# Optimization experiments

Hardware: AMD Instinct MI355X
Metric: run time of the kernel (lower is better)

The kernel has to match this reference:

```python
import jax, jax.numpy as jnp
from jax import lax
import numpy as np

# model dims
N, CIN, T = 4, 1, 8000
C = 256      # encoder/bottleneck channels
D = 512      # dconv_size
K = 3        # residual kernel size
FK, FS = 20, 10  # front kernel / stride
REPEATS, BLOCKS = 4, 8
NB = REPEATS * BLOCKS
EPS = 1e-5
DN = ('NCH', 'OIH', 'NCH')


def setup_inputs() -> dict:
    key = jax.random.key(0)
    ks = jax.random.split(key, 20)
    rn = lambda k, s, sc=0.05: (jax.random.normal(k, s, dtype=jnp.float32) * sc)
    inp = {
        'x': jax.random.normal(ks[0], (N, CIN, T), dtype=jnp.float32),
        'w_enc': rn(ks[1], (C, CIN, FK), 0.2),
        'w1': rn(ks[2], (NB, D, C, 1)),
        'wd': rn(ks[3], (NB, D, 1, K), 0.2),
        'w2': rn(ks[4], (NB, C, D, 1)),
        'w_dec': rn(ks[5], (C, CIN, FK), 0.2),
    }
    # BatchNorm params (inference-style): bn1 over C, bn2/bn3 over D
    for name, ch, base in (('bn1', C, 6), ('bn2', D, 10), ('bn3', D, 14)):
        inp[name + '_g'] = 1.0 + rn(ks[base + 0], (NB, ch), 0.1)
        inp[name + '_b'] = rn(ks[base + 1], (NB, ch), 0.1)
        inp[name + '_m'] = rn(ks[base + 2], (NB, ch), 0.1)
        inp[name + '_v'] = 0.5 + jax.random.uniform(ks[base + 3], (NB, ch), dtype=jnp.float32)
    return inp


def _bn(x, g, b, m, v):
    # x: [N, C, L]; per-channel affine normalization (eval-mode BatchNorm1d)
    scale = g / jnp.sqrt(v + EPS)
    return x * scale[:, None] + (b - m * scale)[:, None]


def _conv1x1(x, w):
    # x: [N, Ci, L], w: [Co, Ci, 1]
    return jnp.einsum('ncl,oc->nol', x, w[:, :, 0])


def reference(x, w_enc, w1, wd, w2, w_dec,
              bn1_g, bn1_b, bn1_m, bn1_v,
              bn2_g, bn2_b, bn2_m, bn2_v,
              bn3_g, bn3_b, bn3_m, bn3_v):
    time = x.shape[2]
    # encoder: Conv1d(CIN->C, k=FK, stride=FS, padding=FK)
    xe = lax.conv_general_dilated(x, w_enc, (FS,), [(FK, FK)], dimension_numbers=DN)
    h = xe
    for i in range(NB):
        dil = 2 ** (i % BLOCKS)
        pad = dil * (K - 1) // 2
        r = _bn(h, bn1_g[i], bn1_b[i], bn1_m[i], bn1_v[i])
        r = _conv1x1(r, w1[i])                      # [N, D, L]
        r = _bn(r, bn2_g[i], bn2_b[i], bn2_m[i], bn2_v[i])
        r = lax.conv_general_dilated(r, wd[i], (1,), [(pad, pad)],
                                     rhs_dilation=(dil,), dimension_numbers=DN,
                                     feature_group_count=D)
        r = _bn(r, bn3_g[i], bn3_b[i], bn3_m[i], bn3_v[i])
        r = _conv1x1(r, w2[i])                      # [N, C, L]
        h = h + r
    mask = jax.nn.sigmoid(h)
    y = xe * mask
    # ConvTranspose1d(C->CIN, k=FK, stride=FS, padding=0)
    wk = jnp.flip(jnp.swapaxes(w_dec, 0, 1), -1)     # [CIN, C, FK]
    out = lax.conv_general_dilated(y, wk, (1,), [(FK - 1, FK - 1)],
                                   lhs_dilation=(FS,), dimension_numbers=DN)
    return out[:, :, FK:time + FK]
```

## Files before the change

kernel.cpp:

```cpp
#include <hip/hip_runtime.h>
#include <cstddef>
#include <cstring>

#define T_     8000
#define L_     803
#define C_     256
#define D_     512
#define NB_    32
#define FK_    20
#define NBATCH 4
#define EPS_   1e-5f

#define NVALID 208
#define NGRID  224
#define NTHR   512
#define SG     1040

typedef __attribute__((ext_vector_type(8))) short bf16x8;
typedef __attribute__((ext_vector_type(4))) short shortx4;
typedef __attribute__((ext_vector_type(4))) float f32x4;
typedef unsigned long long u64;

__device__ __forceinline__ short f2bf(float x) {
  unsigned u = __float_as_uint(x);
  u += 0x7FFF + ((u >> 16) & 1);
  return (short)(u >> 16);
}
__device__ __forceinline__ float bf2f(short u) {
  return __uint_as_float(((unsigned)(unsigned short)u) << 16);
}

__device__ __forceinline__ void astore8(void* p, u64 v) {
  __hip_atomic_store((u64*)p, v, __ATOMIC_RELAXED, __HIP_MEMORY_SCOPE_AGENT);
}

struct __align__(64) Bar { unsigned cnt; unsigned phase; unsigned pad[14]; };

__device__ __forceinline__ void bar_heavy(Bar* b, unsigned nblk, int tid) {
  __syncthreads();
  if (tid == 0) {
    __threadfence();
    unsigned ph = __hip_atomic_load(&b->phase, __ATOMIC_RELAXED, __HIP_MEMORY_SCOPE_AGENT);
    unsigned prev = __hip_atomic_fetch_add(&b->cnt, 1u, __ATOMIC_RELAXED, __HIP_MEMORY_SCOPE_AGENT);
    if (prev == nblk - 1) {
      __hip_atomic_store(&b->cnt, 0u, __ATOMIC_RELAXED, __HIP_MEMORY_SCOPE_AGENT);
      __hip_atomic_store(&b->phase, ph + 1u, __ATOMIC_RELEASE, __HIP_MEMORY_SCOPE_AGENT);
    } else {
      while (__hip_atomic_load(&b->phase, __ATOMIC_RELAXED, __HIP_MEMORY_SCOPE_AGENT) == ph)
        __builtin_amdgcn_s_sleep(2);
    }
    __threadfence();
  }
  __syncthreads();
}

struct KParams {
  const float *x, *w_enc, *w1, *wd, *w2, *w_dec;
  const float *g1, *bb1, *m1, *v1;
  const float *g2, *bb2, *m2, *v2;
  const float *g3, *bb3, *m3, *v3;
  float *out;
  float *s1, *o1, *s2, *o2, *s3, *o3;
  float *yb;
  short *w1b, *w2b;
  unsigned short *zg;
  unsigned short *b1b;
  unsigned *ct;
  Bar *gbar;
};

__global__ __launch_bounds__(256) void prep_kernel(KParams p) {
  const int gtid = blockIdx.x * 256 + threadIdx.x;
  const int stride = gridDim.x * 256;
  for (int i = gtid; i < NB_ * C_; i += stride) {
    float s = p.g1[i] * rsqrtf(p.v1[i] + EPS_);
    p.s1[i] = s; p.o1[i] = p.bb1[i] - p.m1[i] * s;
  }
  for (int i = gtid; i < NB_ * D_; i += stride) {
    float s2 = p.g2[i] * rsqrtf(p.v2[i] + EPS_);
    p.s2[i] = s2; p.o2[i] = p.bb2[i] - p.m2[i] * s2;
    float s3 = p.g3[i] * rsqrtf(p.v3[i] + EPS_);
    p.s3[i] = s3; p.o3[i] = p.bb3[i] - p.m3[i] * s3;
  }
  for (int i = gtid; i < NB_ * D_ * C_ / 4; i += stride) {
    float4 a = ((const float4*)p.w1)[i];
    float4 b = ((const float4*)p.w2)[i];
    shortx4 sa, sb;
    sa[0] = f2bf(a.x); sa[1] = f2bf(a.y); sa[2] = f2bf(a.z); sa[3] = f2bf(a.w);
    sb[0] = f2bf(b.x); sb[1] = f2bf(b.y); sb[2] = f2bf(b.z); sb[3] = f2bf(b.w);
    *(shortx4*)&p.w1b[4 * i] = sa;
    *(shortx4*)&p.w2b[4 * i] = sb;
  }
}

__global__ __launch_bounds__(NTHR) void tasnet_fused(KParams p) {
  const int tid = threadIdx.x;
  const int bid = blockIdx.x;

  const int r8 = bid & 7, t8 = bid >> 3;
  const int g = (t8 >> 2) * 8 + r8;
  const int y = t8 & 3;
  if (g >= 52) return;
  const int vid = g * 4 + y;
  const int xt = g % 13, n = g / 13;
  const int l0 = xt * 64;

  const int lane = tid & 63, wv = tid >> 6;
  const int frow = lane & 15, kg = lane >> 4;
  const int cw = wv & 3;
  const int ch = wv >> 2;
  const int cbase = y * 64 + cw * 16 + kg * 4;

  __shared__ __align__(16) char BsRaw[64 * SG];
  __shared__ __align__(16) char ZsRaw[64 * SG];

  const size_t B1B = (size_t)NBATCH * L_ * C_;
  const size_t ZB = (size_t)52 * 64 * 512;

  f32x4 hreg[2], xer[2];
  {
    const float* xn_ = p.x + (size_t)n * T_;
#pragma unroll
    for (int jb = 0; jb < 2; ++jb) {
      int gl = l0 + ch * 32 + jb * 16 + frow;
      int t0 = gl * 10 - 20;
      float xw[FK_];
#pragma unroll
      for (int k = 0; k < FK_; ++k) {
        int t = t0 + k;
        xw[k] = (t >= 0 && t < T_) ? xn_[t] : 0.f;
      }
#pragma unroll
      for (int jj = 0; jj < 4; ++jj) {
        const float* w = p.w_enc + (cbase + jj) * FK_;
        float acc = 0.f;
#pragma unroll
        for (int k = 0; k < FK_; ++k) acc = fmaf(xw[k], w[k], acc);
        hreg[jb][jj] = acc;
        xer[jb][jj] = acc;
      }
    }
    unsigned short* b0 = p.b1b + (size_t)n * (L_ * C_);
    float4 s1v = *(const float4*)(p.s1 + cbase);
    float4 o1v = *(const float4*)(p.o1 + cbase);
#pragma unroll
    for (int jb = 0; jb < 2; ++jb) {
      int gl = l0 + ch * 32 + jb * 16 + frow;
      if (gl < L_) {
        shortx4 pk;
        pk[0] = f2bf(fmaf(hreg[jb][0], s1v.x, o1v.x));
        pk[1] = f2bf(fmaf(hreg[jb][1], s1v.y, o1v.y));
        pk[2] = f2bf(fmaf(hreg[jb][2], s1v.z, o1v.z));
        pk[3] = f2bf(fmaf(hreg[jb][3], s1v.w, o1v.w));
        *(shortx4*)(b0 + (size_t)gl * C_ + cbase) = pk;
      }
    }
  }
  __syncthreads();
  if (tid == 0)
    __hip_atomic_store(&p.ct[vid], 2u, __ATOMIC_RELAXED, __HIP_MEMORY_SCOPE_AGENT);

  for (int layer = 0; layer < NB_; ++layer) {
    const int dil = 1 << (layer & 7);
    const int step = (dil <= 64) ? 1 : 2;
    const float* s1p = p.s1 + layer * C_;
    const float* o1p = p.o1 + layer * C_;
    const float* s2p = p.s2 + layer * D_;
    const float* o2p = p.o2 + layer * D_;
    const float* s3p = p.s3 + layer * D_;
    const float* o3p = p.o3 + layer * D_;
    const unsigned short* b1_cur = p.b1b + (size_t)layer * B1B + (size_t)n * (L_ * C_);
    unsigned short* b1_nxt = p.b1b + (size_t)(layer + 1) * B1B + (size_t)n * (L_ * C_);
    unsigned short* zstrip = p.zg + (size_t)layer * ZB + (size_t)(n * 13 + xt) * (64 * 512);

    {
      float4 s1v = *(const float4*)(s1p + cbase);
      float4 o1v = *(const float4*)(o1p + cbase);
#pragma unroll
      for (int jb = 0; jb < 2; ++jb) {
        int col = ch * 32 + jb * 16 + frow;
        shortx4 pk;
        pk[0] = f2bf(fmaf(hreg[jb][0], s1v.x, o1v.x));
        pk[1] = f2bf(fmaf(hreg[jb][1], s1v.y, o1v.y));
        pk[2] = f2bf(fmaf(hreg[jb][2], s1v.z, o1v.z));
        pk[3] = f2bf(fmaf(hreg[jb][3], s1v.w, o1v.w));
        *(shortx4*)(BsRaw + (cbase >> 3) * SG + col * 16 + (kg & 1) * 8) = pk;
      }
    }
    if (wv == 0 && lane < 3) {
      int idx = g * 4 + ((y + 1 + lane) & 3);
      unsigned tgt = 2u + 2u * (unsigned)layer;
      while (__hip_atomic_load(&p.ct[idx], __ATOMIC_RELAXED, __HIP_MEMORY_SCOPE_AGENT) < tgt)
        __builtin_amdgcn_s_sleep(1);
    }
    __syncthreads();
    {
      int col = tid >> 3, k8 = tid & 7;
      int gl = l0 + col;
      bool lv = gl < L_;
#pragma unroll
      for (int s = 1; s < 4; ++s) {
        int sc = ((y + s) & 3) * 64 + k8 * 8;
        bf16x8 pk = {0, 0, 0, 0, 0, 0, 0, 0};
        if (lv) pk = *(const bf16x8*)(b1_cur + (size_t)gl * C_ + sc);
        *(bf16x8*)(BsRaw + (sc >> 3) * SG + col * 16) = pk;
      }
    }
    __syncthreads();

    f32x4 acc1[4] = {};
    {
      const short* W1 = p.w1b + (size_t)layer * D_ * C_ + (size_t)(y * 128 + wv * 16 + frow) * C_;
#pragma unroll
      for (int k0 = 0; k0 < 8; ++k0) {
        int kb = k0 * 32 + kg * 8;
        bf16x8 af = *(const bf16x8*)(W1 + kb);
#pragma unroll
        for (int jb = 0; jb < 4; ++jb) {
          bf16x8 bfr = *(bf16x8*)(BsRaw + (k0 * 4 + kg) * SG + (jb * 16 + frow) * 16);
          acc1[jb] = __builtin_amdgcn_mfma_f32_16x16x32_bf16(af, bfr, acc1[jb], 0, 0, 0);
        }
      }
    }
    {
      const int w = (dil < 64) ? dil : 64;
      const int rdL = xt - step, rdR = xt + step;
      const bool pubL = (rdL >= 0);
      const bool pubR = (rdR <= 12);
      int db = y * 128 + wv * 16 + kg * 4;
      float4 s2v = *(const float4*)(s2p + db);
      float4 o2v = *(const float4*)(o2p + db);
#pragma unroll
      for (int jb = 0; jb < 4; ++jb) {
        int col = jb * 16 + frow;
        shortx4 pk;
        pk[0] = f2bf(fmaf(acc1[jb][0], s2v.x, o2v.x));
        pk[1] = f2bf(fmaf(acc1[jb][1], s2v.y, o2v.y));
        pk[2] = f2bf(fmaf(acc1[jb][2], s2v.z, o2v.z));
        pk[3] = f2bf(fmaf(acc1[jb][3], s2v.w, o2v.w));
        *(shortx4*)(ZsRaw + (db >> 3) * SG + col * 16 + (kg & 1) * 8) = pk;
        unsigned short* dst = zstrip + (size_t)col * 512 + db;
        bool haloL = pubL && (col < w);
        bool haloR = pubR && (col >= 64 - w);
        if (haloL || haloR) {
          u64 u;
          __builtin_memcpy(&u, &pk, 8);
          astore8(dst, u);
        } else {
          *(shortx4*)dst = pk;
        }
      }
    }
    __syncthreads();
    if (tid == 0)
      __hip_atomic_store(&p.ct[vid], (unsigned)(2 * layer + 3),
                         __ATOMIC_RELAXED, __HIP_MEMORY_SCOPE_AGENT);
    if (wv == 0 && lane < 11) {
      int idx = -1;
      if (lane < 3) idx = g * 4 + ((y + 1 + lane) & 3);
      else {
        int k = lane - 3;
        int xn2 = xt + ((k >> 2) ? step : -step);
        if (xn2 >= 0 && xn2 <= 12) idx = (n * 13 + xn2) * 4 + (k & 3);
      }
      if (idx >= 0) {
        unsigned tgt = (unsigned)(2 * layer + 3);
        while (__hip_atomic_load(&p.ct[idx], __ATOMIC_RELAXED, __HIP_MEMORY_SCOPE_AGENT) < tgt)
          __builtin_amdgcn_s_sleep(1);
      }
    }
    __syncthreads();
    {
      int col = tid >> 3, k8 = tid & 7;
#pragma unroll
      for (int s = 1; s < 4; ++s) {
        int sd0g = ((y + s) & 3) * 16;
#pragma unroll
        for (int q = 0; q < 2; ++q) {
          int dg = sd0g + k8 * 2 + q;
          bf16x8 zv = *(const bf16x8*)(zstrip + (size_t)col * 512 + dg * 8);
          *(bf16x8*)(ZsRaw + dg * SG + col * 16) = zv;
        }
      }
    }
    __syncthreads();

    {
      const float* wdp = p.wd + (size_t)layer * D_ * 3 + lane * 24;
      float4 wq[6];
#pragma unroll
      for (int q = 0; q < 6; ++q) wq[q] = *(const float4*)(wdp + 4 * q);
      float4 s3a = *(const float4*)(s3p + lane * 8), s3b = *(const float4*)(s3p + lane * 8 + 4);
      float4 o3a = *(const float4*)(o3p + lane * 8), o3b = *(const float4*)(o3p + lane * 8 + 4);
      const unsigned short* zlay = p.zg + (size_t)layer * ZB;
#pragma unroll
      for (int rr = 0; rr < 8; ++rr) {
        int row = wv * 8 + rr;
        int gcol = l0 + row;
        bf16x8 zc = *(bf16x8*)(ZsRaw + lane * SG + row * 16);
        bf16x8 zl = {0, 0, 0, 0, 0, 0, 0, 0};
        bf16x8 zr = {0, 0, 0, 0, 0, 0, 0, 0};
        int gl2 = gcol - dil, gr2 = gcol + dil;
        if (gl2 >= 0) {
          if (gl2 >= l0) zl = *(bf16x8*)(ZsRaw + lane * SG + (gl2 - l0) * 16);
          else zl = *(const bf16x8*)(zlay + (size_t)(n * 13 + (gl2 >> 6)) * (64 * 512)
                                     + (size_t)(gl2 & 63) * 512 + lane * 8);
        }
        if (gr2 < L_) {
          if (gr2 < l0 + 64) zr = *(bf16x8*)(ZsRaw + lane * SG + (gr2 - l0) * 16);
          else zr = *(const bf16x8*)(zlay + (size_t)(n * 13 + (gr2 >> 6)) * (64 * 512)
                                     + (size_t)(gr2 & 63) * 512 + lane * 8);
        }
        bf16x8 pb;
#pragma unroll
        for (int j = 0; j < 8; ++j) {
          float w0 = wq[(3 * j + 0) >> 2][(3 * j + 0) & 3];
          float w1v = wq[(3 * j + 1) >> 2][(3 * j + 1) & 3];
          float w2v = wq[(3 * j + 2) >> 2][(3 * j + 2) & 3];
          float m = bf2f(zc[j]) * w1v;
          m = fmaf(bf2f(zl[j]), w0, m);
          m = fmaf(bf2f(zr[j]), w2v, m);
          float s3v = (j < 4) ? s3a[j] : s3b[j - 4];
          float o3v = (j < 4) ? o3a[j] : o3b[j - 4];
          pb[j] = f2bf(fmaf(m, s3v, o3v));
        }
        *(bf16x8*)(BsRaw + lane * SG + row * 16) = pb;
      }
    }
    __syncthreads();

    {
      f32x4 acc2[2] = {};
      const short* W2 = p.w2b + (size_t)layer * C_ * D_ + (size_t)(y * 64 + cw * 16 + frow) * D_;
#pragma unroll
      for (int k0 = 0; k0 < 16; ++k0) {
        int kb = k0 * 32 + kg * 8;
        bf16x8 af = *(const bf16x8*)(W2 + kb);
#pragma unroll
        for (int jb = 0; jb < 2; ++jb) {
          int col = ch * 32 + jb * 16 + frow;
          bf16x8 bfr = *(bf16x8*)(BsRaw + (k0 * 4 + kg) * SG + col * 16);
          acc2[jb] = __builtin_amdgcn_mfma_f32_16x16x32_bf16(af, bfr, acc2[jb], 0, 0, 0);
        }
      }
#pragma unroll
      for (int jb = 0; jb < 2; ++jb)
#pragma unroll
        for (int jj = 0; jj < 4; ++jj)
          hreg[jb][jj] += acc2[jb][jj];
    }
    if (layer + 1 < NB_) {
      float4 s1v = *(const float4*)(p.s1 + (layer + 1) * C_ + cbase);
      float4 o1v = *(const float4*)(p.o1 + (layer + 1) * C_ + cbase);
#pragma unroll
      for (int jb = 0; jb < 2; ++jb) {
        int gl = l0 + ch * 32 + jb * 16 + frow;
        if (gl < L_) {
          shortx4 pk;
          pk[0] = f2bf(fmaf(hreg[jb][0], s1v.x, o1v.x));
          pk[1] = f2bf(fmaf(hreg[jb][1], s1v.y, o1v.y));
          pk[2] = f2bf(fmaf(hreg[jb][2], s1v.z, o1v.z));
          pk[3] = f2bf(fmaf(hreg[jb][3], s1v.w, o1v.w));
          *(shortx4*)(b1_nxt + (size_t)gl * C_ + cbase) = pk;
        }
      }
    }
    __syncthreads();
    if (tid == 0)
      __hip_atomic_store(&p.ct[vid], (unsigned)(2 * layer + 4),
                         __ATOMIC_RELAXED, __HIP_MEMORY_SCOPE_AGENT);
  }

  {
    float* yn = p.yb + (size_t)n * ((size_t)L_ * C_);
#pragma unroll
    for (int jb = 0; jb < 2; ++jb) {
      int gl = l0 + ch * 32 + jb * 16 + frow;
      if (gl < L_) {
        float4 v;
        v.x = xer[jb][0] / (1.f + expf(-hreg[jb][0]));
        v.y = xer[jb][1] / (1.f + expf(-hreg[jb][1]));
        v.z = xer[jb][2] / (1.f + expf(-hreg[jb][2]));
        v.w = xer[jb][3] / (1.f + expf(-hreg[jb][3]));
        *(float4*)(yn + (size_t)gl * C_ + cbase) = v;
      }
    }
  }
  bar_heavy(p.gbar, NVALID, tid);

  for (int idx = vid * NTHR + tid; idx < NBATCH * T_; idx += NVALID * NTHR) {
    int t = idx % T_;
    int nn = idx / T_;
    int tt = t + FK_;
    int lq = tt / 10;
    int k0 = tt % 10;
    const float* y0 = p.yb + (size_t)nn * ((size_t)L_ * C_) + (size_t)lq * C_;
    const float* y1 = y0 - C_;
    float acc = 0.f;
#pragma unroll 8
    for (int c = 0; c < C_; c++) {
      const float* wr2 = p.w_dec + c * FK_;
      acc = fmaf(y0[c], wr2[k0], acc);
      acc = fmaf(y1[c], wr2[k0 + 10], acc);
    }
    p.out[idx] = acc;
  }
}

extern "C" void kernel_launch(void* const* d_in, const int* in_sizes, int n_in,
                              void* d_out, int out_size, void* d_ws, size_t ws_size,
                              hipStream_t stream) {
  KParams hp;
  hp.x     = (const float*)d_in[0];
  hp.w_enc = (const float*)d_in[1];
  hp.w1    = (const float*)d_in[2];
  hp.wd    = (const float*)d_in[3];
  hp.w2    = (const float*)d_in[4];
  hp.w_dec = (const float*)d_in[5];
  hp.g1 = (const float*)d_in[6];  hp.bb1 = (const float*)d_in[7];
  hp.m1 = (const float*)d_in[8];  hp.v1  = (const float*)d_in[9];
  hp.g2 = (const float*)d_in[10]; hp.bb2 = (const float*)d_in[11];
  hp.m2 = (const float*)d_in[12]; hp.v2  = (const float*)d_in[13];
  hp.g3 = (const float*)d_in[14]; hp.bb3 = (const float*)d_in[15];
  hp.m3 = (const float*)d_in[16]; hp.v3  = (const float*)d_in[17];
  hp.out = (float*)d_out;

  char* cur = (char*)d_ws;
  auto take = [&](size_t bytes) { char* r = cur; cur += (bytes + 255) & ~(size_t)255; return r; };
  hp.gbar = (Bar*)take(256);
  hp.ct   = (unsigned*)take(NVALID * 4);
  hp.s1 = (float*)take(NB_ * C_ * 4);
  hp.o1 = (float*)take(NB_ * C_ * 4);
  hp.s2 = (float*)take(NB_ * D_ * 4);
  hp.o2 = (float*)take(NB_ * D_ * 4);
  hp.s3 = (float*)take(NB_ * D_ * 4);
  hp.o3 = (float*)take(NB_ * D_ * 4);
  hp.yb  = (float*)take((size_t)NBATCH * L_ * C_ * 4);
  hp.w1b = (short*)take((size_t)NB_ * D_ * C_ * 2);
  hp.w2b = (short*)take((size_t)NB_ * D_ * C_ * 2);
  hp.b1b = (unsigned short*)take((size_t)NB_ * NBATCH * L_ * C_ * 2);
  hp.zg  = (unsigned short*)take((size_t)NB_ * 52 * 64 * 512 * 2);

  hipMemsetAsync(d_ws, 0, 2048, stream);
  prep_kernel<<<dim3(1024), dim3(256), 0, stream>>>(hp);
  tasnet_fused<<<dim3(NGRID), dim3(NTHR), 0, stream>>>(hp);
}
```

Measured before the change: 556.0 us.

## Split depthwise conv across D-quarter blocks and exchange post-conv activations

Previously each of the four blocks sharing a 64-column tile gathered the full 512-channel z strip from peers and each computed the whole depthwise conv redundantly. Now each block keeps only its own 128-channel z slice in shared memory, publishes only halo columns, and computes the depthwise conv plus BN3 for its own channels. It then exchanges the bf16 results with its three siblings through a global buffer before the second 1x1 GEMM. Interior columns are computed before the wait on neighbor halos, so that work can overlap the wait. This removes redundant depthwise compute and the full-strip z traffic, in exchange for an extra synchronization phase per layer and a new counter scheme.

```diff
diff --git a/kernel.cpp b/kernel.cpp
--- a/kernel.cpp
+++ b/kernel.cpp
@@ -63,7 +63,8 @@
   float *s1, *o1, *s2, *o2, *s3, *o3;
   float *yb;
   short *w1b, *w2b;
-  unsigned short *zg;
+  unsigned short *zh;
+  unsigned short *b3g;
   unsigned short *b1b;
   unsigned *ct;
   Bar *gbar;
@@ -112,10 +113,11 @@
   const int cbase = y * 64 + cw * 16 + kg * 4;
 
   __shared__ __align__(16) char BsRaw[64 * SG];
-  __shared__ __align__(16) char ZsRaw[64 * SG];
+  __shared__ __align__(16) char ZsOwn[16 * SG];
 
   const size_t B1B = (size_t)NBATCH * L_ * C_;
-  const size_t ZB = (size_t)52 * 64 * 512;
+  const size_t ZHB = (size_t)52 * 4 * 64 * 128;
+  const size_t B3B = (size_t)52 * 64 * 512;
 
   f32x4 hreg[2], xer[2];
   {
@@ -158,11 +160,12 @@
   }
   __syncthreads();
   if (tid == 0)
-    __hip_atomic_store(&p.ct[vid], 2u, __ATOMIC_RELAXED, __HIP_MEMORY_SCOPE_AGENT);
+    __hip_atomic_store(&p.ct[vid], 1u, __ATOMIC_RELAXED, __HIP_MEMORY_SCOPE_AGENT);
 
   for (int layer = 0; layer < NB_; ++layer) {
     const int dil = 1 << (layer & 7);
     const int step = (dil <= 64) ? 1 : 2;
+    const int w = (dil < 64) ? dil : 64;
     const float* s1p = p.s1 + layer * C_;
     const float* o1p = p.o1 + layer * C_;
     const float* s2p = p.s2 + layer * D_;
@@ -171,7 +174,10 @@
     const float* o3p = p.o3 + layer * D_;
     const unsigned short* b1_cur = p.b1b + (size_t)layer * B1B + (size_t)n * (L_ * C_);
     unsigned short* b1_nxt = p.b1b + (size_t)(layer + 1) * B1B + (size_t)n * (L_ * C_);
-    unsigned short* zstrip = p.zg + (size_t)layer * ZB + (size_t)(n * 13 + xt) * (64 * 512);
+    unsigned short* zh_my = p.zh + (size_t)layer * ZHB
+                            + ((size_t)(n * 13 + xt) * 4 + y) * (64 * 128);
+    unsigned short* b3s = p.b3g + (size_t)(layer & 15) * B3B
+                          + (size_t)(n * 13 + xt) * (64 * 512);
 
     {
       float4 s1v = *(const float4*)(s1p + cbase);
@@ -189,7 +195,7 @@
     }
     if (wv == 0 && lane < 3) {
       int idx = g * 4 + ((y + 1 + lane) & 3);
-      unsigned tgt = 2u + 2u * (unsigned)layer;
+      unsigned tgt = (unsigned)(3 * layer + 1);
       while (__hip_atomic_load(&p.ct[idx], __ATOMIC_RELAXED, __HIP_MEMORY_SCOPE_AGENT) < tgt)
         __builtin_amdgcn_s_sleep(1);
     }
@@ -223,13 +229,11 @@
       }
     }
     {
-      const int w = (dil < 64) ? dil : 64;
-      const int rdL = xt - step, rdR = xt + step;
-      const bool pubL = (rdL >= 0);
-      const bool pubR = (rdR <= 12);
-      int db = y * 128 + wv * 16 + kg * 4;
-      float4 s2v = *(const float4*)(s2p + db);
-      float4 o2v = *(const float4*)(o2p + db);
+      const bool hasL = (xt - step) >= 0;
+      const bool hasR = (xt + step) <= 12;
+      int dbr = wv * 16 + kg * 4;
+      float4 s2v = *(const float4*)(s2p + y * 128 + dbr);
+      float4 o2v = *(const float4*)(o2p + y * 128 + dbr);
 #pragma unroll
       for (int jb = 0; jb < 4; ++jb) {
         int col = jb * 16 + frow;
@@ -238,93 +242,107 @@
         pk[1] = f2bf(fmaf(acc1[jb][1], s2v.y, o2v.y));
         pk[2] = f2bf(fmaf(acc1[jb][2], s2v.z, o2v.z));
         pk[3] = f2bf(fmaf(acc1[jb][3], s2v.w, o2v.w));
-        *(shortx4*)(ZsRaw + (db >> 3) * SG + col * 16 + (kg & 1) * 8) = pk;
-        unsigned short* dst = zstrip + (size_t)col * 512 + db;
-        bool haloL = pubL && (col < w);
-        bool haloR = pubR && (col >= 64 - w);
+        *(shortx4*)(ZsOwn + (dbr >> 3) * SG + col * 16 + (kg & 1) * 8) = pk;
+        bool haloL = hasL && (col < w);
+        bool haloR = hasR && (col >= 64 - w);
         if (haloL || haloR) {
           u64 u;
           __builtin_memcpy(&u, &pk, 8);
-          astore8(dst, u);
-        } else {
-          *(shortx4*)dst = pk;
+          astore8(zh_my + (size_t)col * 128 + dbr, u);
         }
       }
     }
     __syncthreads();
     if (tid == 0)
-      __hip_atomic_store(&p.ct[vid], (unsigned)(2 * layer + 3),
+      __hip_atomic_store(&p.ct[vid], (unsigned)(3 * layer + 2),
                          __ATOMIC_RELAXED, __HIP_MEMORY_SCOPE_AGENT);
-    if (wv == 0 && lane < 11) {
-      int idx = -1;
-      if (lane < 3) idx = g * 4 + ((y + 1 + lane) & 3);
-      else {
-        int k = lane - 3;
-        int xn2 = xt + ((k >> 2) ? step : -step);
-        if (xn2 >= 0 && xn2 <= 12) idx = (n * 13 + xn2) * 4 + (k & 3);
-      }
-      if (idx >= 0) {
-        unsigned tgt = (unsigned)(2 * layer + 3);
-        while (__hip_atomic_load(&p.ct[idx], __ATOMIC_RELAXED, __HIP_MEMORY_SCOPE_AGENT) < tgt)
-          __builtin_amdgcn_s_sleep(1);
-      }
+
+    {
+      const int col = tid >> 3;
+      const int op = tid & 7;
+      const int gcol = l0 + col;
+      const int gl2 = gcol - dil, gr2 = gcol + dil;
+      const bool remL = (gl2 >= 0) && (gl2 < l0);
+      const bool remR = (gr2 < L_) && (gr2 >= l0 + 64);
+      const bool isRem = remL || remR;
+      const unsigned short* zhl = p.zh + (size_t)layer * ZHB;
+#pragma unroll
+      for (int pass = 0; pass < 2; ++pass) {
+        if (pass == 1) {
+          if (wv == 0 && lane < 2) {
+            int xn2 = xt + ((lane == 0) ? -step : step);
+            if (xn2 >= 0 && xn2 <= 12) {
+              int idx = (n * 13 + xn2) * 4 + y;
+              unsigned tgt = (unsigned)(3 * layer + 2);
+              while (__hip_atomic_load(&p.ct[idx], __ATOMIC_RELAXED, __HIP_MEMORY_SCOPE_AGENT) < tgt)
+                __builtin_amdgcn_s_sleep(1);
+            }
+          }
+          __syncthreads();
+        }
+        if ((pass == 0) == isRem) continue;
+#pragma unroll
+        for (int oc = 0; oc < 2; ++oc) {
+          int drel = op * 16 + oc * 8;
+          int dglob = y * 128 + drel;
+          const float* wdp = p.wd + (size_t)layer * D_ * 3 + dglob * 3;
+          float4 wq[6];
+#pragma unroll
+          for (int q = 0; q < 6; ++q) wq[q] = *(const float4*)(wdp + 4 * q);
+          float4 s3a = *(const float4*)(s3p + dglob), s3b = *(const float4*)(s3p + dglob + 4);
+          float4 o3a = *(const float4*)(o3p + dglob), o3b = *(const float4*)(o3p + dglob + 4);
+          bf16x8 zc = *(bf16x8*)(ZsOwn + (drel >> 3) * SG + col * 16);
+          bf16x8 zl = {0, 0, 0, 0, 0, 0, 0, 0};
+          bf16x8 zr = {0, 0, 0, 0, 0, 0, 0, 0};
+          if (gl2 >= 0) {
+            if (!remL) zl = *(bf16x8*)(ZsOwn + (drel >> 3) * SG + (gl2 - l0) * 16);
+            else zl = *(const bf16x8*)(zhl + ((size_t)(n * 13 + (gl2 >> 6)) * 4 + y) * (64 * 128)
+                                       + (size_t)(gl2 & 63) * 128 + drel);
+          }
+          if (gr2 < L_) {
+            if (!remR) zr = *(bf16x8*)(ZsOwn + (drel >> 3) * SG + (gr2 - l0) * 16);
+            else zr = *(const bf16x8*)(zhl + ((size_t)(n * 13 + (gr2 >> 6)) * 4 + y) * (64 * 128)
+                                       + (size_t)(gr2 & 63) * 128 + drel);
+          }
+          bf16x8 pb;
+#pragma unroll
+          for (int j = 0; j < 8; ++j) {
+            float w0v = wq[(3 * j + 0) >> 2][(3 * j + 0) & 3];
+            float w1v = wq[(3 * j + 1) >> 2][(3 * j + 1) & 3];
+            float w2v = wq[(3 * j + 2) >> 2][(3 * j + 2) & 3];
+            float m = bf2f(zc[j]) * w1v;
+            m = fmaf(bf2f(zl[j]), w0v, m);
+            m = fmaf(bf2f(zr[j]), w2v, m);
+            float s3v = (j < 4) ? s3a[j] : s3b[j - 4];
+            float o3v = (j < 4) ? o3a[j] : o3b[j - 4];
+            pb[j] = f2bf(fmaf(m, s3v, o3v));
+          }
+          *(bf16x8*)(BsRaw + (y * 16 + (drel >> 3)) * SG + col * 16) = pb;
+          *(bf16x8*)(b3s + (size_t)col * 512 + dglob) = pb;
+        }
+      }
+    }
+    __syncthreads();
+    if (tid == 0)
+      __hip_atomic_store(&p.ct[vid], (unsigned)(3 * layer + 3),
+                         __ATOMIC_RELAXED, __HIP_MEMORY_SCOPE_AGENT);
+    if (wv == 0 && lane < 3) {
+      int idx = g * 4 + ((y + 1 + lane) & 3);
+      unsigned tgt = (unsigned)(3 * layer + 3);
+      while (__hip_atomic_load(&p.ct[idx], __ATOMIC_RELAXED, __HIP_MEMORY_SCOPE_AGENT) < tgt)
+        __builtin_amdgcn_s_sleep(1);
     }
     __syncthreads();
     {
       int col = tid >> 3, k8 = tid & 7;
 #pragma unroll
       for (int s = 1; s < 4; ++s) {
-        int sd0g = ((y + s) & 3) * 16;
-#pragma unroll
-        for (int q = 0; q < 2; ++q) {
-          int dg = sd0g + k8 * 2 + q;
-          bf16x8 zv = *(const bf16x8*)(zstrip + (size_t)col * 512 + dg * 8);
-          *(bf16x8*)(ZsRaw + dg * SG + col * 16) = zv;
-        }
-      }
-    }
-    __syncthreads();
-
-    {
-      const float* wdp = p.wd + (size_t)layer * D_ * 3 + lane * 24;
-      float4 wq[6];
-#pragma unroll
-      for (int q = 0; q < 6; ++q) wq[q] = *(const float4*)(wdp + 4 * q);
-      float4 s3a = *(const float4*)(s3p + lane * 8), s3b = *(const float4*)(s3p + lane * 8 + 4);
-      float4 o3a = *(const float4*)(o3p + lane * 8), o3b = *(const float4*)(o3p + lane * 8 + 4);
-      const unsigned short* zlay = p.zg + (size_t)layer * ZB;
-#pragma unroll
-      for (int rr = 0; rr < 8; ++rr) {
-        int row = wv * 8 + rr;
-        int gcol = l0 + row;
-        bf16x8 zc = *(bf16x8*)(ZsRaw + lane * SG + row * 16);
-        bf16x8 zl = {0, 0, 0, 0, 0, 0, 0, 0};
-        bf16x8 zr = {0, 0, 0, 0, 0, 0, 0, 0};
-        int gl2 = gcol - dil, gr2 = gcol + dil;
-        if (gl2 >= 0) {
-          if (gl2 >= l0) zl = *(bf16x8*)(ZsRaw + lane * SG + (gl2 - l0) * 16);
-          else zl = *(const bf16x8*)(zlay + (size_t)(n * 13 + (gl2 >> 6)) * (64 * 512)
-                                     + (size_t)(gl2 & 63) * 512 + lane * 8);
-        }
-        if (gr2 < L_) {
-          if (gr2 < l0 + 64) zr = *(bf16x8*)(ZsRaw + lane * SG + (gr2 - l0) * 16);
-          else zr = *(const bf16x8*)(zlay + (size_t)(n * 13 + (gr2 >> 6)) * (64 * 512)
-                                     + (size_t)(gr2 & 63) * 512 + lane * 8);
-        }
-        bf16x8 pb;
-#pragma unroll
-        for (int j = 0; j < 8; ++j) {
-          float w0 = wq[(3 * j + 0) >> 2][(3 * j + 0) & 3];
-          float w1v = wq[(3 * j + 1) >> 2][(3 * j + 1) & 3];
-          float w2v = wq[(3 * j + 2) >> 2][(3 * j + 2) & 3];
-          float m = bf2f(zc[j]) * w1v;
-          m = fmaf(bf2f(zl[j]), w0, m);
-          m = fmaf(bf2f(zr[j]), w2v, m);
-          float s3v = (j < 4) ? s3a[j] : s3b[j - 4];
-          float o3v = (j < 4) ? o3a[j] : o3b[j - 4];
-          pb[j] = f2bf(fmaf(m, s3v, o3v));
-        }
-        *(bf16x8*)(BsRaw + lane * SG + row * 16) = pb;
+        int y2 = (y + s) & 3;
+        const unsigned short* src = b3s + (size_t)col * 512 + y2 * 128 + k8 * 16;
+        bf16x8 v0 = *(const bf16x8*)(src);
+        bf16x8 v1 = *(const bf16x8*)(src + 8);
+        *(bf16x8*)(BsRaw + (y2 * 16 + k8 * 2) * SG + col * 16) = v0;
+        *(bf16x8*)(BsRaw + (y2 * 16 + k8 * 2 + 1) * SG + col * 16) = v1;
       }
     }
     __syncthreads();
@@ -367,7 +385,7 @@
     }
     __syncthreads();
     if (tid == 0)
-      __hip_atomic_store(&p.ct[vid], (unsigned)(2 * layer + 4),
+      __hip_atomic_store(&p.ct[vid], (unsigned)(3 * layer + 4),
                          __ATOMIC_RELAXED, __HIP_MEMORY_SCOPE_AGENT);
   }
 
@@ -439,7 +457,8 @@
   hp.w1b = (short*)take((size_t)NB_ * D_ * C_ * 2);
   hp.w2b = (short*)take((size_t)NB_ * D_ * C_ * 2);
   hp.b1b = (unsigned short*)take((size_t)NB_ * NBATCH * L_ * C_ * 2);
-  hp.zg  = (unsigned short*)take((size_t)NB_ * 52 * 64 * 512 * 2);
+  hp.b3g = (unsigned short*)take((size_t)16 * 52 * 64 * 512 * 2);
+  hp.zh  = (unsigned short*)take((size_t)NB_ * 52 * 4 * 64 * 128 * 2);
 
   hipMemsetAsync(d_ws, 0, 2048, stream);
   prep_kernel<<<dim3(1024), dim3(256), 0, stream>>>(hp);
```

Result: faster. 516.2 us (-7.2%).
